# Kernel optimization log

Measured on AMD Instinct MI355X. Metric: run time of the kernel, lower is better.

The kernel has to match this reference:

```python
import jax, jax.numpy as jnp
import numpy as np

B, LQ, LK = 16, 1024, 2048
E, F, A = 512, 256, 512


def setup_inputs() -> dict:
    key = jax.random.key(0)
    ks = jax.random.split(key, 8)
    s_e = 1.0 / np.sqrt(E)
    s_f = 1.0 / np.sqrt(F)
    s_a = 1.0 / np.sqrt(A)
    return {
        "lstm_embeddings": jax.random.normal(ks[0], (B, LQ, E), jnp.float32),
        "optical_flow_features": jax.random.normal(ks[1], (B, LK, F), jnp.float32),
        "Wq": jax.random.normal(ks[2], (E, A), jnp.float32) * s_e,
        "bq": jnp.zeros((A,), jnp.float32),
        "Wk": jax.random.normal(ks[3], (F, A), jnp.float32) * s_f,
        "bk": jnp.zeros((A,), jnp.float32),
        "Wv": jax.random.normal(ks[4], (F, A), jnp.float32) * s_f,
        "bv": jnp.zeros((A,), jnp.float32),
        "Wo": jax.random.normal(ks[5], (A, E), jnp.float32) * s_a,
        "bo": jnp.zeros((E,), jnp.float32),
    }


def reference(lstm_embeddings, optical_flow_features, Wq, bq, Wk, bk, Wv, bv, Wo, bo):
    # Linear projections (x @ W + b), matching nn.Linear with W stored as [in, out]
    q = lstm_embeddings @ Wq + bq            # [B, LQ, A]
    k = optical_flow_features @ Wk + bk      # [B, LK, A]
    v = optical_flow_features @ Wv + bv      # [B, LK, A]
    # NOTE: original module does NOT scale scores by 1/sqrt(A) — stay faithful.
    scores = jnp.einsum("bqa,bka->bqk", q, k)      # [B, LQ, LK]
    weights = jax.nn.softmax(scores, axis=-1)
    context = jnp.einsum("bqk,bka->bqa", weights, v)  # [B, LQ, A]
    return context @ Wo + bo                          # [B, LQ, E]
```

## Files before the change

### kernel.cpp

```cpp
#include <hip/hip_runtime.h>


#define DEV static __device__ __forceinline__

typedef __attribute__((ext_vector_type(8))) short s8v;
typedef __attribute__((ext_vector_type(8))) _Float16 h8v;
typedef __attribute__((ext_vector_type(4))) _Float16 h4v;
typedef __attribute__((ext_vector_type(4))) float f4v;
typedef __attribute__((ext_vector_type(16))) float f16f;
typedef __attribute__((ext_vector_type(4))) float float4v;
typedef unsigned short u16;
typedef unsigned int u32;

constexpr int BB = 16;
constexpr int LQ = 1024;
constexpr int LK = 2048;
constexpr int E = 512;
constexpr int F = 256;

DEV u16 f2bf(float x) {
    u32 u = __builtin_bit_cast(u32, x);
    u += 0x7fff + ((u >> 16) & 1);
    return (u16)(u >> 16);
}
DEV float bf2f(u16 h) { return __builtin_bit_cast(float, (u32)h << 16); }

DEV f4v MF(s8v a, s8v b, f4v c) {
    return __builtin_amdgcn_mfma_f32_16x16x32_bf16(a, b, c, 0, 0, 0);
}
DEV f4v MF16(h8v a, h8v b, f4v c) {
    return __builtin_amdgcn_mfma_f32_16x16x32_f16(a, b, c, 0, 0, 0);
}
DEV f16f MF32(h8v a, h8v b, f16f c) {
    return __builtin_amdgcn_mfma_f32_32x32x16_f16(a, b, c, 0, 0, 0);
}

DEV void gll16(const _Float16* g, _Float16* l) {
    __builtin_amdgcn_global_load_lds(
        (const __attribute__((address_space(1))) u32*)g,
        (__attribute__((address_space(3))) u32*)l, 16, 0, 0);
}

__global__ __launch_bounds__(256) void prew(
    const float* __restrict__ y, _Float16* __restrict__ yA,
    _Float16* __restrict__ yB,
    const float* __restrict__ Wq, const float* __restrict__ bq,
    const float* __restrict__ Wk, const float* __restrict__ Wv,
    const float* __restrict__ bv, const float* __restrict__ Wo,
    const float* __restrict__ bo,
    u16* __restrict__ Mhb, u16* __restrict__ Ntb,
    float* __restrict__ wvec, float* __restrict__ cvec)
{
    __shared__ __align__(16) char smem[33536];
    const int tid = threadIdx.x;
    const int bi = blockIdx.x;

    if (bi < 1024) {
        float (*Y)[260] = (float(*)[260])smem;
        const int b = bi >> 6, t = bi & 63;
        const float* src = y + ((size_t)b * LK + t * 32) * F;
#pragma unroll
        for (int i = 0; i < 8; ++i) {
            int base = i * 1024 + tid * 4;
            int k = base >> 8, f = base & 255;
            *(float4v*)&Y[k][f] = *(const float4v*)(src + base);
        }
        __syncthreads();
        size_t tb = (size_t)(b * 64 + t) * 8192;
#pragma unroll
        for (int i = 0; i < 4; ++i) {
            int c = i * 256 + tid;
            int k = c & 31, hi = (c >> 5) & 1, fs = c >> 6;
            int f0 = fs * 16 + hi * 8;
            float4v v0 = *(const float4v*)&Y[k][f0];
            float4v v1 = *(const float4v*)&Y[k][f0 + 4];
            h8v v;
#pragma unroll
            for (int j = 0; j < 4; ++j) { v[j] = (_Float16)v0[j]; v[4 + j] = (_Float16)v1[j]; }
            *(h8v*)(yA + tb + (size_t)c * 8) = v;
        }
#pragma unroll
        for (int i = 0; i < 4; ++i) {
            int c = i * 256 + tid;
            int fl = c & 31, hi = (c >> 5) & 1, frag = c >> 6;
            int ft = frag >> 1, ks = frag & 1;
            int f = ft * 32 + fl, k0 = ks * 16 + hi * 8;
            h8v v;
#pragma unroll
            for (int j = 0; j < 8; ++j) v[j] = (_Float16)Y[k0 + j][f];
            *(h8v*)(yB + tb + (size_t)c * 8) = v;
        }
        return;
    }

    const int wb = bi - 1024;
    if (wb >= 64) {
        if (wb == 64) {
            const float* r = Wk + (size_t)tid * 512;
            float s = 0.f;
#pragma unroll 4
            for (int a = 0; a < 512; a += 4) {
                float4v v = *(const float4v*)(r + a);
                float4v bb = *(const float4v*)(bq + a);
                s += v[0] * bb[0] + v[1] * bb[1] + v[2] * bb[2] + v[3] * bb[3];
            }
            wvec[tid] = s;
        } else {
            int e = (wb - 65) * 256 + tid;
            float s = bo[e];
#pragma unroll 4
            for (int a = 0; a < 512; ++a) s += bv[a] * Wo[(size_t)a * 512 + e];
            cvec[e] = s;
        }
        return;
    }

    const bool ntm = wb >= 32;
    const int bj = ntm ? wb - 32 : wb;
    const int m0 = ntm ? (bj >> 2) * 64 : (bj >> 3) * 64;
    const int n0 = ntm ? (bj & 3) * 64 : (bj & 7) * 64;
    const float* Ag = ntm ? Wo : Wk;
    const float* Bg = ntm ? Wv : Wq;

    u16 (*Ash)[40] = (u16(*)[40])(smem);
    u16 (*Asl)[40] = (u16(*)[40])(smem + 5120);
    u16 (*Bsh)[40] = (u16(*)[40])(smem + 10240);
    u16 (*Bsl)[40] = (u16(*)[40])(smem + 15360);

    const int w = tid >> 6, lane = tid & 63;
    const int g = lane >> 4, qn = lane & 15;
    const int wr = w & 1, wc = w >> 1;

    f4v acc[2][2];
#pragma unroll
    for (int i = 0; i < 2; ++i)
#pragma unroll
        for (int j = 0; j < 2; ++j) acc[i][j] = (f4v){0.f, 0.f, 0.f, 0.f};

    for (int k0 = 0; k0 < 512; k0 += 32) {
        __syncthreads();
        if (!ntm) {
            int r = tid & 63, c = (tid >> 6) * 8;
            const float* s = Ag + (size_t)(m0 + r) * 512 + k0 + c;
            float4v v0 = *(const float4v*)s, v1 = *(const float4v*)(s + 4);
            short hh[8], ll[8];
#pragma unroll
            for (int i = 0; i < 8; ++i) {
                float x = (i < 4) ? v0[i] : v1[i - 4];
                u16 h = f2bf(x);
                hh[i] = (short)h;
                ll[i] = (short)f2bf(x - bf2f(h));
            }
            *(s8v*)&Ash[r][c] = (s8v){hh[0],hh[1],hh[2],hh[3],hh[4],hh[5],hh[6],hh[7]};
            *(s8v*)&Asl[r][c] = (s8v){ll[0],ll[1],ll[2],ll[3],ll[4],ll[5],ll[6],ll[7]};
        } else {
            int k = tid >> 3, mc = (tid & 7) * 8;
            const float* s = Ag + (size_t)(k0 + k) * 512 + m0 + mc;
            float4v v0 = *(const float4v*)s, v1 = *(const float4v*)(s + 4);
#pragma unroll
            for (int i = 0; i < 8; ++i) {
                float x = (i < 4) ? v0[i] : v1[i - 4];
                u16 h = f2bf(x);
                Ash[mc + i][k] = h;
                Asl[mc + i][k] = f2bf(x - bf2f(h));
            }
        }
        {
            int r = tid & 63, c = (tid >> 6) * 8;
            const float* s = Bg + (size_t)(n0 + r) * 512 + k0 + c;
            float4v v0 = *(const float4v*)s, v1 = *(const float4v*)(s + 4);
            short hh[8], ll[8];
#pragma unroll
            for (int i = 0; i < 8; ++i) {
                float x = (i < 4) ? v0[i] : v1[i - 4];
                u16 h = f2bf(x);
                hh[i] = (short)h;
                ll[i] = (short)f2bf(x - bf2f(h));
            }
            *(s8v*)&Bsh[r][c] = (s8v){hh[0],hh[1],hh[2],hh[3],hh[4],hh[5],hh[6],hh[7]};
            *(s8v*)&Bsl[r][c] = (s8v){ll[0],ll[1],ll[2],ll[3],ll[4],ll[5],ll[6],ll[7]};
        }
        __syncthreads();

        s8v ah[2], al[2], bh[2], bl[2];
#pragma unroll
        for (int mt = 0; mt < 2; ++mt) {
            ah[mt] = *(const s8v*)&Ash[wr * 32 + mt * 16 + qn][g * 8];
            al[mt] = *(const s8v*)&Asl[wr * 32 + mt * 16 + qn][g * 8];
        }
#pragma unroll
        for (int nt = 0; nt < 2; ++nt) {
            bh[nt] = *(const s8v*)&Bsh[wc * 32 + nt * 16 + qn][g * 8];
            bl[nt] = *(const s8v*)&Bsl[wc * 32 + nt * 16 + qn][g * 8];
        }
#pragma unroll
        for (int mt = 0; mt < 2; ++mt)
#pragma unroll
            for (int nt = 0; nt < 2; ++nt) {
                acc[mt][nt] = MF(ah[mt], bh[nt], acc[mt][nt]);
                acc[mt][nt] = MF(ah[mt], bl[nt], acc[mt][nt]);
                acc[mt][nt] = MF(al[mt], bh[nt], acc[mt][nt]);
            }
    }

#pragma unroll
    for (int mt = 0; mt < 2; ++mt)
#pragma unroll
        for (int nt = 0; nt < 2; ++nt)
#pragma unroll
            for (int r = 0; r < 4; ++r) {
                int gm = m0 + wr * 32 + mt * 16 + 4 * g + r;
                int gn = n0 + wc * 32 + nt * 16 + qn;
                float v = acc[mt][nt][r];
                if (!ntm) {
                    size_t off = (size_t)((gn >> 5) * 16 + (gm >> 4)) * 512 +
                                 (gm & 15) * 8 + ((gn >> 3) & 3) * 128 + (gn & 7);
                    Mhb[off] = __builtin_bit_cast(u16, (_Float16)v);
                } else {
                    size_t off = (size_t)((gn >> 5) * 32 + (gm >> 4)) * 512 +
                                 (gm & 15) * 8 + ((gn >> 3) & 3) * 128 + (gn & 7);
                    Ntb[off] = __builtin_bit_cast(u16, (_Float16)v);
                }
            }
}

__global__ __launch_bounds__(256) void qprime6(
    const float* __restrict__ x, const u16* __restrict__ Mhb,
    const float* __restrict__ wv, _Float16* __restrict__ q16)
{
    __shared__ _Float16 Xs[2][64][40];
    const int tid = threadIdx.x, w = tid >> 6, lane = tid & 63;
    const int g = lane >> 4, qn = lane & 15;
    const int m0 = blockIdx.x * 64;
    const int nh = blockIdx.y * 8;
    const int srow = tid >> 2, scol = (tid & 3) * 8;
    const _Float16* Mh = (const _Float16*)Mhb;

    f4v acc[8];
#pragma unroll
    for (int n = 0; n < 8; ++n) acc[n] = (f4v){0.f, 0.f, 0.f, 0.f};

    float4v a0, a1;
    auto LDA = [&](int k0) {
        const float* s = x + (size_t)(m0 + srow) * 512 + k0 + scol;
        a0 = *(const float4v*)s;
        a1 = *(const float4v*)(s + 4);
    };
    auto STA = [&](int buf) {
        h8v v;
#pragma unroll
        for (int j = 0; j < 4; ++j) { v[j] = (_Float16)a0[j]; v[4 + j] = (_Float16)a1[j]; }
        *(h8v*)&Xs[buf][srow][scol] = v;
    };
    h8v b0[8], b1[8];
    auto LDB0 = [&](int t) {
        const int fb = t * 16 + nh;
#pragma unroll
        for (int nt = 0; nt < 8; ++nt)
            b0[nt] = *(const h8v*)(Mh + (size_t)(fb + nt) * 512 + lane * 8);
    };
    auto LDB1 = [&](int t) {
        const int fb = t * 16 + nh;
#pragma unroll
        for (int nt = 0; nt < 8; ++nt)
            b1[nt] = *(const h8v*)(Mh + (size_t)(fb + nt) * 512 + lane * 8);
    };

    LDA(0); STA(0); LDA(32); LDB0(0);
    __syncthreads();

#pragma unroll
    for (int t = 0; t < 16; ++t) {
        const int cur = t & 1;
        if (t < 15) { if (cur == 0) LDB1(t + 1); else LDB0(t + 1); }
        h8v af = *(const h8v*)&Xs[cur][w * 16 + qn][g * 8];
        if (cur == 0) {
#pragma unroll
            for (int nt = 0; nt < 8; ++nt) acc[nt] = MF16(af, b0[nt], acc[nt]);
        } else {
#pragma unroll
            for (int nt = 0; nt < 8; ++nt) acc[nt] = MF16(af, b1[nt], acc[nt]);
        }
        if (t < 15) {
            STA(cur ^ 1);
            if (t < 14) LDA((t + 2) * 32);
            __syncthreads();
        }
    }

#pragma unroll
    for (int nt = 0; nt < 8; ++nt) {
        int col = (nh + nt) * 16 + qn;
        float wvc = wv[col];
#pragma unroll
        for (int r = 0; r < 4; ++r) {
            int row = m0 + w * 16 + 4 * g + r;
            q16[(size_t)row * 256 + col] =
                (_Float16)((acc[nt][r] + wvc) * 1.44269504f);
        }
    }
}

__global__ __launch_bounds__(512) void flash8(
    const _Float16* __restrict__ q16, const _Float16* __restrict__ yA,
    const _Float16* __restrict__ yB, _Float16* __restrict__ part,
    float* __restrict__ ml)
{
    __shared__ _Float16 Asb[2][2][8192];
    __shared__ _Float16 Bsb[2][2][8192];
    __shared__ _Float16 Pls[8][1024];

    const int tid = threadIdx.x;
    const int w = tid >> 6, lane = tid & 63;
    const int q32 = lane & 31, hi = lane >> 5;

    int id = blockIdx.x;
    int xcd = id & 7, slot = id >> 3;
    int grp = xcd + 8 * (slot >> 2);
    int qb = slot & 3;
    int b = grp >> 2, z = grp & 3;
    const int qw = qb * 256 + w * 32;

    h8v qf[16];
    {
        const _Float16* qp = q16 + ((size_t)b * LQ + qw + q32) * 256 + hi * 8;
#pragma unroll
        for (int s = 0; s < 16; ++s) qf[s] = *(const h8v*)(qp + s * 16);
    }
    f16f ctx[8];
#pragma unroll
    for (int i = 0; i < 8; ++i) ctx[i] = (f16f){};
    float mrun = -3.0e38f, lrun = 0.f;

    const size_t tbe = (size_t)(b * 64 + z * 16) * 8192;

    auto STAGE = [&](int sup, int buf) {
#pragma unroll
        for (int j = 0; j < 2; ++j) {
            const _Float16* ga = yA + tbe + (size_t)(sup * 2 + j) * 8192 + tid * 8;
            const _Float16* gb = yB + tbe + (size_t)(sup * 2 + j) * 8192 + tid * 8;
            gll16(ga,        &Asb[buf][j][tid * 8]);
            gll16(ga + 4096, &Asb[buf][j][tid * 8 + 4096]);
            gll16(gb,        &Bsb[buf][j][tid * 8]);
            gll16(gb + 4096, &Bsb[buf][j][tid * 8 + 4096]);
        }
    };

    STAGE(0, 0);
    __syncthreads();

    int buf = 0;
    for (int s = 0; s < 8; ++s) {
        if (s < 7) STAGE(s + 1, buf ^ 1);
#pragma unroll
        for (int j = 0; j < 2; ++j) {
            const _Float16* Ap = &Asb[buf][j][0];
            const _Float16* Bp = &Bsb[buf][j][0];
            f16f S = (f16f){};
#pragma unroll
            for (int fs = 0; fs < 16; ++fs) {
                h8v a = *(const h8v*)(Ap + fs * 512 + lane * 8);
                S = MF32(a, qf[fs], S);
            }
            float mt = S[0];
#pragma unroll
            for (int r = 1; r < 16; ++r) mt = fmaxf(mt, S[r]);
            mt = fmaxf(mt, __shfl_xor(mt, 32));
            if (!__all(mt <= mrun + 11.5416f)) {
                float mnew = fmaxf(mrun, mt);
                float alpha = exp2f(mrun - mnew);
                lrun *= alpha;
#pragma unroll
                for (int r = 0; r < 16; ++r) {
                    int qr = (r & 3) + 8 * (r >> 2) + 4 * hi;
                    float ar = __shfl(alpha, qr);
#pragma unroll
                    for (int ft = 0; ft < 8; ++ft) ctx[ft][r] *= ar;
                }
                mrun = mnew;
            }
            float p[16], ps = 0.f;
#pragma unroll
            for (int r = 0; r < 16; ++r) { p[r] = exp2f(S[r] - mrun); ps += p[r]; }
            ps += __shfl_xor(ps, 32);
            lrun += ps;
            {
                _Float16* pw = &Pls[w][0];
#pragma unroll
                for (int r2 = 0; r2 < 4; ++r2) {
                    h4v pk = (h4v){(_Float16)p[4 * r2], (_Float16)p[4 * r2 + 1],
                                   (_Float16)p[4 * r2 + 2], (_Float16)p[4 * r2 + 3]};
                    *(h4v*)(pw + (r2 >> 1) * 512 + (r2 & 1) * 256 + q32 * 8 + hi * 4) = pk;
                }
            }
#pragma unroll
            for (int ks = 0; ks < 2; ++ks) {
                h8v pa = *(const h8v*)(&Pls[w][ks * 512] + lane * 8);
#pragma unroll
                for (int ft = 0; ft < 8; ++ft) {
                    h8v bf = *(const h8v*)(Bp + (ft * 2 + ks) * 512 + lane * 8);
                    ctx[ft] = MF32(pa, bf, ctx[ft]);
                }
            }
        }
        __syncthreads();
        buf ^= 1;
    }

    float linv = 1.f / lrun;
    _Float16* pp = part + ((size_t)z * (BB * LQ) + (size_t)b * LQ + qw) * 256;
#pragma unroll
    for (int r = 0; r < 16; ++r) {
        int qr = (r & 3) + 8 * (r >> 2) + 4 * hi;
        float ir = __shfl(linv, qr);
#pragma unroll
        for (int ft = 0; ft < 8; ++ft)
            pp[(size_t)qr * 256 + ft * 32 + q32] = (_Float16)(ctx[ft][r] * ir);
    }
    if (hi == 0) {
        size_t mi = (size_t)z * (BB * LQ) + (size_t)b * LQ + qw + q32;
        ml[2 * mi + 0] = mrun;
        ml[2 * mi + 1] = lrun;
    }
}

__global__ __launch_bounds__(256) void gemm2c2(
    const _Float16* __restrict__ part, const float* __restrict__ ml,
    const u16* __restrict__ Ntb, const float* __restrict__ cvec,
    float* __restrict__ out)
{
    __shared__ _Float16 Asb[32][40];
    __shared__ float scl[32][4];
    const int tid = threadIdx.x;
    const int w = tid >> 6, lane = tid & 63;
    const int g = lane >> 4, qn = lane & 15;
    const int m0 = blockIdx.x * 32;
    constexpr size_t PL = (size_t)BB * LQ * F;
    constexpr size_t PR = (size_t)BB * LQ;

    if (tid < 32) {
        size_t i = m0 + tid;
        float m0v = ml[2 * i], l0v = ml[2 * i + 1];
        float m1v = ml[2 * (PR + i)], l1v = ml[2 * (PR + i) + 1];
        float m2v = ml[2 * (2 * PR + i)], l2v = ml[2 * (2 * PR + i) + 1];
        float m3v = ml[2 * (3 * PR + i)], l3v = ml[2 * (3 * PR + i) + 1];
        float M = fmaxf(fmaxf(m0v, m1v), fmaxf(m2v, m3v));
        float e0v = exp2f(m0v - M), e1v = exp2f(m1v - M);
        float e2v = exp2f(m2v - M), e3v = exp2f(m3v - M);
        float inv = 1.f / (l0v * e0v + l1v * e1v + l2v * e2v + l3v * e3v);
        scl[tid][0] = l0v * e0v * inv;
        scl[tid][1] = l1v * e1v * inv;
        scl[tid][2] = l2v * e2v * inv;
        scl[tid][3] = l3v * e3v * inv;
    }

    f4v acc[2][8];
#pragma unroll
    for (int i = 0; i < 2; ++i)
#pragma unroll
        for (int j = 0; j < 8; ++j) acc[i][j] = (f4v){0.f, 0.f, 0.f, 0.f};

    for (int k0 = 0; k0 < F; k0 += 32) {
        __syncthreads();
        {
            int r = tid >> 3, cc = (tid & 7) * 4;
            size_t base = (size_t)(m0 + r) * F + k0 + cc;
            h4v p0 = *(const h4v*)(part + base);
            h4v p1 = *(const h4v*)(part + PL + base);
            h4v p2 = *(const h4v*)(part + 2 * PL + base);
            h4v p3 = *(const h4v*)(part + 3 * PL + base);
            float s0 = scl[r][0], s1 = scl[r][1], s2 = scl[r][2], s3 = scl[r][3];
#pragma unroll
            for (int i = 0; i < 4; ++i) {
                float v = (float)p0[i] * s0 + (float)p1[i] * s1 +
                          (float)p2[i] * s2 + (float)p3[i] * s3;
                Asb[r][cc + i] = (_Float16)v;
            }
        }
        __syncthreads();

        h8v ah[2];
#pragma unroll
        for (int mt = 0; mt < 2; ++mt)
            ah[mt] = *(const h8v*)&Asb[mt * 16 + qn][g * 8];
#pragma unroll
        for (int nt = 0; nt < 8; ++nt) {
            h8v bh = *(const h8v*)((const _Float16*)Ntb +
                     (size_t)((k0 >> 5) * 32 + w * 8 + nt) * 512 + lane * 8);
            acc[0][nt] = MF16(ah[0], bh, acc[0][nt]);
            acc[1][nt] = MF16(ah[1], bh, acc[1][nt]);
        }
    }

#pragma unroll
    for (int mt = 0; mt < 2; ++mt)
#pragma unroll
        for (int nt = 0; nt < 8; ++nt)
#pragma unroll
            for (int r = 0; r < 4; ++r) {
                int gm = m0 + mt * 16 + 4 * g + r;
                int gn = w * 128 + nt * 16 + qn;
                out[(size_t)gm * E + gn] = acc[mt][nt][r] + cvec[gn];
            }
}

extern "C" void kernel_launch(void* const* d_in, const int* in_sizes, int n_in,
                              void* d_out, int out_size, void* d_ws, size_t ws_size,
                              hipStream_t stream)
{
    const float* x  = (const float*)d_in[0];
    const float* y  = (const float*)d_in[1];
    const float* Wq = (const float*)d_in[2];
    const float* bq = (const float*)d_in[3];
    const float* Wk = (const float*)d_in[4];
    const float* Wv = (const float*)d_in[6];
    const float* bv = (const float*)d_in[7];
    const float* Wo = (const float*)d_in[8];
    const float* bo = (const float*)d_in[9];
    float* out = (float*)d_out;

    char* ws = (char*)d_ws;
    size_t off = 0;
    auto alloc = [&](size_t bytes) -> char* {
        char* p = ws + off;
        off = (off + bytes + 255) & ~(size_t)255;
        return p;
    };
    u16* Mhb  = (u16*)alloc(sizeof(u16) * F * E);
    float* wvec = (float*)alloc(sizeof(float) * F);
    float* cvec = (float*)alloc(sizeof(float) * E);
    u16* Ntb  = (u16*)alloc(sizeof(u16) * E * F);
    _Float16* q16 = (_Float16*)alloc(sizeof(u16) * (size_t)BB * LQ * F);
    _Float16* yA  = (_Float16*)alloc(sizeof(u16) * (size_t)BB * LK * F);
    _Float16* yB  = (_Float16*)alloc(sizeof(u16) * (size_t)BB * LK * F);
    _Float16* part = (_Float16*)alloc(sizeof(u16) * 4 * (size_t)BB * LQ * F);
    float* ml = (float*)alloc(sizeof(float) * 2 * 4 * (size_t)BB * LQ);
    (void)ws_size; (void)in_sizes; (void)n_in; (void)out_size;

    prew<<<dim3(1091), dim3(256), 0, stream>>>(
        y, yA, yB, Wq, bq, Wk, Wv, bv, Wo, bo, Mhb, Ntb, wvec, cvec);
    qprime6<<<dim3(BB * LQ / 64, 2), dim3(256), 0, stream>>>(x, Mhb, wvec, q16);
    flash8<<<dim3(256), dim3(512), 0, stream>>>(q16, yA, yB, part, ml);
    gemm2c2<<<dim3(BB * LQ / 32), dim3(256), 0, stream>>>(
        part, ml, Ntb, cvec, out);
}
```

Measured before the change: 135.7 us.

## Move y conversion into q-projection kernel and switch softmax to natural exp

Splits the weight-preprocessing kernel so the small weight GEMMs run alone. The fp16 conversion and reordering of the optical-flow features now share a launch with the query projection, to balance work across the kernel boundary. The log2(e) prescale on q is dropped, and the softmax uses __expf with an equivalent rescale threshold. That may add a multiply per exponent in the flash loop.

```diff
diff --git a/kernel.cpp b/kernel.cpp
--- a/kernel.cpp
+++ b/kernel.cpp
@@ -41,9 +41,7 @@
         (__attribute__((address_space(3))) u32*)l, 16, 0, 0);
 }
 
-__global__ __launch_bounds__(256) void prew(
-    const float* __restrict__ y, _Float16* __restrict__ yA,
-    _Float16* __restrict__ yB,
+__global__ __launch_bounds__(256) void wgemm(
     const float* __restrict__ Wq, const float* __restrict__ bq,
     const float* __restrict__ Wk, const float* __restrict__ Wv,
     const float* __restrict__ bv, const float* __restrict__ Wo,
@@ -51,51 +49,10 @@
     u16* __restrict__ Mhb, u16* __restrict__ Ntb,
     float* __restrict__ wvec, float* __restrict__ cvec)
 {
-    __shared__ __align__(16) char smem[33536];
+    const int bi = blockIdx.x;
     const int tid = threadIdx.x;
-    const int bi = blockIdx.x;
-
-    if (bi < 1024) {
-        float (*Y)[260] = (float(*)[260])smem;
-        const int b = bi >> 6, t = bi & 63;
-        const float* src = y + ((size_t)b * LK + t * 32) * F;
-#pragma unroll
-        for (int i = 0; i < 8; ++i) {
-            int base = i * 1024 + tid * 4;
-            int k = base >> 8, f = base & 255;
-            *(float4v*)&Y[k][f] = *(const float4v*)(src + base);
-        }
-        __syncthreads();
-        size_t tb = (size_t)(b * 64 + t) * 8192;
-#pragma unroll
-        for (int i = 0; i < 4; ++i) {
-            int c = i * 256 + tid;
-            int k = c & 31, hi = (c >> 5) & 1, fs = c >> 6;
-            int f0 = fs * 16 + hi * 8;
-            float4v v0 = *(const float4v*)&Y[k][f0];
-            float4v v1 = *(const float4v*)&Y[k][f0 + 4];
-            h8v v;
-#pragma unroll
-            for (int j = 0; j < 4; ++j) { v[j] = (_Float16)v0[j]; v[4 + j] = (_Float16)v1[j]; }
-            *(h8v*)(yA + tb + (size_t)c * 8) = v;
-        }
-#pragma unroll
-        for (int i = 0; i < 4; ++i) {
-            int c = i * 256 + tid;
-            int fl = c & 31, hi = (c >> 5) & 1, frag = c >> 6;
-            int ft = frag >> 1, ks = frag & 1;
-            int f = ft * 32 + fl, k0 = ks * 16 + hi * 8;
-            h8v v;
-#pragma unroll
-            for (int j = 0; j < 8; ++j) v[j] = (_Float16)Y[k0 + j][f];
-            *(h8v*)(yB + tb + (size_t)c * 8) = v;
-        }
-        return;
-    }
-
-    const int wb = bi - 1024;
-    if (wb >= 64) {
-        if (wb == 64) {
+    if (bi >= 64) {
+        if (bi == 64) {
             const float* r = Wk + (size_t)tid * 512;
             float s = 0.f;
 #pragma unroll 4
@@ -106,7 +63,7 @@
             }
             wvec[tid] = s;
         } else {
-            int e = (wb - 65) * 256 + tid;
+            int e = (bi - 65) * 256 + tid;
             float s = bo[e];
 #pragma unroll 4
             for (int a = 0; a < 512; ++a) s += bv[a] * Wo[(size_t)a * 512 + e];
@@ -115,17 +72,15 @@
         return;
     }
 
-    const bool ntm = wb >= 32;
-    const int bj = ntm ? wb - 32 : wb;
+    __shared__ u16 Ash[64][40], Asl[64][40];
+    __shared__ u16 Bsh[64][40], Bsl[64][40];
+
+    const bool ntm = bi >= 32;
+    const int bj = ntm ? bi - 32 : bi;
     const int m0 = ntm ? (bj >> 2) * 64 : (bj >> 3) * 64;
     const int n0 = ntm ? (bj & 3) * 64 : (bj & 7) * 64;
     const float* Ag = ntm ? Wo : Wk;
     const float* Bg = ntm ? Wv : Wq;
-
-    u16 (*Ash)[40] = (u16(*)[40])(smem);
-    u16 (*Asl)[40] = (u16(*)[40])(smem + 5120);
-    u16 (*Bsh)[40] = (u16(*)[40])(smem + 10240);
-    u16 (*Bsl)[40] = (u16(*)[40])(smem + 15360);
 
     const int w = tid >> 6, lane = tid & 63;
     const int g = lane >> 4, qn = lane & 15;
@@ -224,84 +179,130 @@
             }
 }
 
-__global__ __launch_bounds__(256) void qprime6(
+__global__ __launch_bounds__(256) void prepq(
+    const float* __restrict__ y, _Float16* __restrict__ yA,
+    _Float16* __restrict__ yB,
     const float* __restrict__ x, const u16* __restrict__ Mhb,
     const float* __restrict__ wv, _Float16* __restrict__ q16)
 {
-    __shared__ _Float16 Xs[2][64][40];
-    const int tid = threadIdx.x, w = tid >> 6, lane = tid & 63;
-    const int g = lane >> 4, qn = lane & 15;
-    const int m0 = blockIdx.x * 64;
-    const int nh = blockIdx.y * 8;
-    const int srow = tid >> 2, scol = (tid & 3) * 8;
-    const _Float16* Mh = (const _Float16*)Mhb;
-
-    f4v acc[8];
-#pragma unroll
-    for (int n = 0; n < 8; ++n) acc[n] = (f4v){0.f, 0.f, 0.f, 0.f};
-
-    float4v a0, a1;
-    auto LDA = [&](int k0) {
-        const float* s = x + (size_t)(m0 + srow) * 512 + k0 + scol;
-        a0 = *(const float4v*)s;
-        a1 = *(const float4v*)(s + 4);
-    };
-    auto STA = [&](int buf) {
-        h8v v;
-#pragma unroll
-        for (int j = 0; j < 4; ++j) { v[j] = (_Float16)a0[j]; v[4 + j] = (_Float16)a1[j]; }
-        *(h8v*)&Xs[buf][srow][scol] = v;
-    };
-    h8v b0[8], b1[8];
-    auto LDB0 = [&](int t) {
-        const int fb = t * 16 + nh;
-#pragma unroll
-        for (int nt = 0; nt < 8; ++nt)
-            b0[nt] = *(const h8v*)(Mh + (size_t)(fb + nt) * 512 + lane * 8);
-    };
-    auto LDB1 = [&](int t) {
-        const int fb = t * 16 + nh;
-#pragma unroll
-        for (int nt = 0; nt < 8; ++nt)
-            b1[nt] = *(const h8v*)(Mh + (size_t)(fb + nt) * 512 + lane * 8);
-    };
-
-    LDA(0); STA(0); LDA(32); LDB0(0);
-    __syncthreads();
-
-#pragma unroll
-    for (int t = 0; t < 16; ++t) {
-        const int cur = t & 1;
-        if (t < 15) { if (cur == 0) LDB1(t + 1); else LDB0(t + 1); }
-        h8v af = *(const h8v*)&Xs[cur][w * 16 + qn][g * 8];
-        if (cur == 0) {
-#pragma unroll
-            for (int nt = 0; nt < 8; ++nt) acc[nt] = MF16(af, b0[nt], acc[nt]);
-        } else {
-#pragma unroll
-            for (int nt = 0; nt < 8; ++nt) acc[nt] = MF16(af, b1[nt], acc[nt]);
-        }
-        if (t < 15) {
-            STA(cur ^ 1);
-            if (t < 14) LDA((t + 2) * 32);
-            __syncthreads();
-        }
-    }
-
-#pragma unroll
-    for (int nt = 0; nt < 8; ++nt) {
-        int col = (nh + nt) * 16 + qn;
-        float wvc = wv[col];
-#pragma unroll
-        for (int r = 0; r < 4; ++r) {
-            int row = m0 + w * 16 + 4 * g + r;
-            q16[(size_t)row * 256 + col] =
-                (_Float16)((acc[nt][r] + wvc) * 1.44269504f);
-        }
-    }
-}
-
-__global__ __launch_bounds__(512) void flash8(
+    __shared__ __align__(16) char smem[33280];
+    const int tid = threadIdx.x;
+    const int bi = blockIdx.x;
+
+    if (bi < 512) {
+        _Float16 (*Xs)[64][40] = (_Float16(*)[64][40])smem;
+        const int w = tid >> 6, lane = tid & 63;
+        const int g = lane >> 4, qn = lane & 15;
+        const int m0 = (bi >> 1) * 64;
+        const int nh = (bi & 1) * 8;
+        const int srow = tid >> 2, scol = (tid & 3) * 8;
+        const _Float16* Mh = (const _Float16*)Mhb;
+
+        f4v acc[8];
+#pragma unroll
+        for (int n = 0; n < 8; ++n) acc[n] = (f4v){0.f, 0.f, 0.f, 0.f};
+
+        float4v a0, a1;
+        auto LDA = [&](int k0) {
+            const float* s = x + (size_t)(m0 + srow) * 512 + k0 + scol;
+            a0 = *(const float4v*)s;
+            a1 = *(const float4v*)(s + 4);
+        };
+        auto STA = [&](int buf) {
+            h8v v;
+#pragma unroll
+            for (int j = 0; j < 4; ++j) { v[j] = (_Float16)a0[j]; v[4 + j] = (_Float16)a1[j]; }
+            *(h8v*)&Xs[buf][srow][scol] = v;
+        };
+        h8v b0[8], b1[8];
+        auto LDB0 = [&](int t) {
+            const int fb = t * 16 + nh;
+#pragma unroll
+            for (int nt = 0; nt < 8; ++nt)
+                b0[nt] = *(const h8v*)(Mh + (size_t)(fb + nt) * 512 + lane * 8);
+        };
+        auto LDB1 = [&](int t) {
+            const int fb = t * 16 + nh;
+#pragma unroll
+            for (int nt = 0; nt < 8; ++nt)
+                b1[nt] = *(const h8v*)(Mh + (size_t)(fb + nt) * 512 + lane * 8);
+        };
+
+        LDA(0); STA(0); LDA(32); LDB0(0);
+        __syncthreads();
+
+#pragma unroll
+        for (int t = 0; t < 16; ++t) {
+            const int cur = t & 1;
+            if (t < 15) { if (cur == 0) LDB1(t + 1); else LDB0(t + 1); }
+            h8v af = *(const h8v*)&Xs[cur][w * 16 + qn][g * 8];
+            if (cur == 0) {
+#pragma unroll
+                for (int nt = 0; nt < 8; ++nt) acc[nt] = MF16(af, b0[nt], acc[nt]);
+            } else {
+#pragma unroll
+                for (int nt = 0; nt < 8; ++nt) acc[nt] = MF16(af, b1[nt], acc[nt]);
+            }
+            if (t < 15) {
+                STA(cur ^ 1);
+                if (t < 14) LDA((t + 2) * 32);
+                __syncthreads();
+            }
+        }
+
+#pragma unroll
+        for (int nt = 0; nt < 8; ++nt) {
+            int col = (nh + nt) * 16 + qn;
+            float wvc = wv[col];
+#pragma unroll
+            for (int r = 0; r < 4; ++r) {
+                int row = m0 + w * 16 + 4 * g + r;
+                q16[(size_t)row * 256 + col] = (_Float16)(acc[nt][r] + wvc);
+            }
+        }
+        return;
+    }
+
+    {
+        const int pb = bi - 512;
+        float (*Y)[260] = (float(*)[260])smem;
+        const int b = pb >> 6, t = pb & 63;
+        const float* src = y + ((size_t)b * LK + t * 32) * F;
+#pragma unroll
+        for (int i = 0; i < 8; ++i) {
+            int base = i * 1024 + tid * 4;
+            int k = base >> 8, f = base & 255;
+            *(float4v*)&Y[k][f] = *(const float4v*)(src + base);
+        }
+        __syncthreads();
+        size_t tb = (size_t)(b * 64 + t) * 8192;
+#pragma unroll
+        for (int i = 0; i < 4; ++i) {
+            int c = i * 256 + tid;
+            int k = c & 31, hi = (c >> 5) & 1, fs = c >> 6;
+            int f0 = fs * 16 + hi * 8;
+            float4v v0 = *(const float4v*)&Y[k][f0];
+            float4v v1 = *(const float4v*)&Y[k][f0 + 4];
+            h8v v;
+#pragma unroll
+            for (int j = 0; j < 4; ++j) { v[j] = (_Float16)v0[j]; v[4 + j] = (_Float16)v1[j]; }
+            *(h8v*)(yA + tb + (size_t)c * 8) = v;
+        }
+#pragma unroll
+        for (int i = 0; i < 4; ++i) {
+            int c = i * 256 + tid;
+            int fl = c & 31, hi = (c >> 5) & 1, frag = c >> 6;
+            int ft = frag >> 1, ks = frag & 1;
+            int f = ft * 32 + fl, k0 = ks * 16 + hi * 8;
+            h8v v;
+#pragma unroll
+            for (int j = 0; j < 8; ++j) v[j] = (_Float16)Y[k0 + j][f];
+            *(h8v*)(yB + tb + (size_t)c * 8) = v;
+        }
+    }
+}
+
+__global__ __launch_bounds__(512) void flash9(
     const _Float16* __restrict__ q16, const _Float16* __restrict__ yA,
     const _Float16* __restrict__ yB, _Float16* __restrict__ part,
     float* __restrict__ ml)
@@ -366,9 +367,9 @@
 #pragma unroll
             for (int r = 1; r < 16; ++r) mt = fmaxf(mt, S[r]);
             mt = fmaxf(mt, __shfl_xor(mt, 32));
-            if (!__all(mt <= mrun + 11.5416f)) {
+            if (!__all(mt <= mrun + 8.f)) {
                 float mnew = fmaxf(mrun, mt);
-                float alpha = exp2f(mrun - mnew);
+                float alpha = __expf(mrun - mnew);
                 lrun *= alpha;
 #pragma unroll
                 for (int r = 0; r < 16; ++r) {
@@ -381,7 +382,7 @@
             }
             float p[16], ps = 0.f;
 #pragma unroll
-            for (int r = 0; r < 16; ++r) { p[r] = exp2f(S[r] - mrun); ps += p[r]; }
+            for (int r = 0; r < 16; ++r) { p[r] = __expf(S[r] - mrun); ps += p[r]; }
             ps += __shfl_xor(ps, 32);
             lrun += ps;
             {
@@ -445,8 +446,8 @@
         float m2v = ml[2 * (2 * PR + i)], l2v = ml[2 * (2 * PR + i) + 1];
         float m3v = ml[2 * (3 * PR + i)], l3v = ml[2 * (3 * PR + i) + 1];
         float M = fmaxf(fmaxf(m0v, m1v), fmaxf(m2v, m3v));
-        float e0v = exp2f(m0v - M), e1v = exp2f(m1v - M);
-        float e2v = exp2f(m2v - M), e3v = exp2f(m3v - M);
+        float e0v = __expf(m0v - M), e1v = __expf(m1v - M);
+        float e2v = __expf(m2v - M), e3v = __expf(m3v - M);
         float inv = 1.f / (l0v * e0v + l1v * e1v + l2v * e2v + l3v * e3v);
         scl[tid][0] = l0v * e0v * inv;
         scl[tid][1] = l1v * e1v * inv;
@@ -537,10 +538,11 @@
     float* ml = (float*)alloc(sizeof(float) * 2 * 4 * (size_t)BB * LQ);
     (void)ws_size; (void)in_sizes; (void)n_in; (void)out_size;
 
-    prew<<<dim3(1091), dim3(256), 0, stream>>>(
-        y, yA, yB, Wq, bq, Wk, Wv, bv, Wo, bo, Mhb, Ntb, wvec, cvec);
-    qprime6<<<dim3(BB * LQ / 64, 2), dim3(256), 0, stream>>>(x, Mhb, wvec, q16);
-    flash8<<<dim3(256), dim3(512), 0, stream>>>(q16, yA, yB, part, ml);
+    wgemm<<<dim3(67), dim3(256), 0, stream>>>(
+        Wq, bq, Wk, Wv, bv, Wo, bo, Mhb, Ntb, wvec, cvec);
+    prepq<<<dim3(1536), dim3(256), 0, stream>>>(
+        y, yA, yB, x, Mhb, wvec, q16);
+    flash9<<<dim3(256), dim3(512), 0, stream>>>(q16, yA, yB, part, ml);
     gemm2c2<<<dim3(BB * LQ / 32), dim3(256), 0, stream>>>(
         part, ml, Ntb, cvec, out);
 }
```

Result: no change. 134.4 us (-1.0%).
